# Optimization experiments

Hardware: AMD Instinct MI355X
Metric: run time of the kernel (lower is better)

## Reference

```python
import jax, jax.numpy as jnp
import numpy as np

NUM_HEADS = 12  # from init_kwargs


def setup_inputs() -> dict:
    key = jax.random.key(0)
    k1, k2, k3 = jax.random.split(key, 3)
    B, N, C = 8, 4096, 768
    x = jax.random.normal(k1, (B, N, C), dtype=jnp.float32)
    qkv_w = jax.random.normal(k2, (3 * C, C), dtype=jnp.float32) * (C ** -0.5)
    proj_w = jax.random.normal(k3, (C, C), dtype=jnp.float32) * (C ** -0.5)
    proj_b = jnp.zeros((C,), dtype=jnp.float32)
    return {"x": x, "qkv_w": qkv_w, "proj_w": proj_w, "proj_b": proj_b}


def reference(x, qkv_w, proj_w, proj_b):
    B, N, C = x.shape
    H = NUM_HEADS
    hd = C // H
    h = w = int(round(N ** 0.5))  # spatial grid, N = h*w
    # fused qkv projection (q, k are produced but never consumed, as in source)
    qkv = jnp.einsum('bnc,dc->bnd', x, qkv_w)          # [B, N, 3C]
    qkv = qkv.reshape(B, N, 3, H, hd)
    v = qkv[:, :, 2].transpose(0, 2, 1, 3)             # [B, H, N, hd]
    v2d = v.reshape(B, H, h, w, hd)
    # fft2 over spatial dims; concat(real, imag) then slice[:hd] == real part
    v_real = jnp.fft.fft2(v2d.astype(jnp.float32), axes=(2, 3)).real
    out = v_real.reshape(B, H, N, hd).transpose(0, 2, 1, 3).reshape(B, N, C)
    return jnp.einsum('bnc,dc->bnd', out, proj_w) + proj_b
```

## Files before the change

### kernel.cpp

```cpp
#include <hip/hip_runtime.h>
#include <hip/hip_bf16.h>


typedef __bf16 bf16x8 __attribute__((ext_vector_type(8)));
typedef __bf16 bf16x4 __attribute__((ext_vector_type(4)));
typedef float f32x4 __attribute__((ext_vector_type(4)));
typedef unsigned short ushort_t;
typedef unsigned int uint_t;

typedef __attribute__((address_space(3))) unsigned int lds_u32;
typedef __attribute__((address_space(1))) unsigned int glob_u32;

__device__ __forceinline__ void gl_lds16(const void* g, void* l) {
  __builtin_amdgcn_global_load_lds((const glob_u32*)g, (lds_u32*)l, 16, 0, 0);
}

__device__ __forceinline__ ushort_t f2bf(float f) {
  union { __hip_bfloat16 h; ushort_t s; } cv;
  cv.h = __float2bfloat16(f);
  return cv.s;
}

__device__ __forceinline__ bf16x8 ld_frag(const ushort_t* p) {
  union { bf16x8 v; bf16x4 h[2]; } r;
  r.h[0] = *(const bf16x4*)p;
  r.h[1] = *(const bf16x4*)(p + 4);
  return r.v;
}

__device__ __forceinline__ bf16x8 tw_frag(int m, int k0, bool use_sin, float sign) {
  union { bf16x8 v; ushort_t u[8]; } r;
#pragma unroll
  for (int j = 0; j < 8; ++j) {
    int ph = (m * (k0 + j)) & 63;
    float a = (float)ph * 0.09817477042468104f;
    float x = use_sin ? __sinf(a) : __cosf(a);
    r.u[j] = f2bf(sign * x);
  }
  return r.v;
}

__global__ __launch_bounds__(256) void precompute_mfma(const float* __restrict__ P,
                                                       const float* __restrict__ Q,
                                                       __hip_bfloat16* __restrict__ Mb) {
  __shared__ ushort_t As[128 * 40];
  __shared__ ushort_t Bs[128 * 36];
  const int t = threadIdx.x;
  const int i0 = blockIdx.y * 128, c0 = blockIdx.x * 128;
  const int w = t >> 6, l = t & 63;
  const int wm = w & 1, wn = w >> 1;
  const int lm = l & 15, lq = l >> 4;
  f32x4 acc[4][4] = {};
  for (int kt = 0; kt < 24; ++kt) {
    const int k0 = kt * 32;
    {
      int e = t * 16, row = e >> 5, dc = e & 16;
      const float* src = &P[(size_t)(i0 + row) * 768 + k0 + dc];
      float4 f0 = *(const float4*)&src[0], f1 = *(const float4*)&src[4];
      float4 f2 = *(const float4*)&src[8], f3 = *(const float4*)&src[12];
      union { ushort_t u[8]; uint4 v; } pk0, pk1;
      pk0.u[0] = f2bf(f0.x); pk0.u[1] = f2bf(f0.y); pk0.u[2] = f2bf(f0.z); pk0.u[3] = f2bf(f0.w);
      pk0.u[4] = f2bf(f1.x); pk0.u[5] = f2bf(f1.y); pk0.u[6] = f2bf(f1.z); pk0.u[7] = f2bf(f1.w);
      pk1.u[0] = f2bf(f2.x); pk1.u[1] = f2bf(f2.y); pk1.u[2] = f2bf(f2.z); pk1.u[3] = f2bf(f2.w);
      pk1.u[4] = f2bf(f3.x); pk1.u[5] = f2bf(f3.y); pk1.u[6] = f2bf(f3.z); pk1.u[7] = f2bf(f3.w);
      *(uint4*)&As[row * 40 + dc] = pk0.v;
      *(uint4*)&As[row * 40 + dc + 8] = pk1.v;
    }
#pragma unroll
    for (int it = 0; it < 8; ++it) {
      int p = it * 256 + t, c = p & 127, pr = p >> 7;
      float a = Q[(size_t)(1536 + k0 + 2 * pr) * 768 + c0 + c];
      float b = Q[(size_t)(1536 + k0 + 2 * pr + 1) * 768 + c0 + c];
      union { ushort_t u[2]; uint_t w_; } pk;
      pk.u[0] = f2bf(a); pk.u[1] = f2bf(b);
      *(uint_t*)&Bs[c * 36 + 2 * pr] = pk.w_;
    }
    __syncthreads();
    bf16x8 af[4], bfr[4];
#pragma unroll
    for (int mt = 0; mt < 4; ++mt)
      af[mt] = ld_frag(&As[(wm * 64 + mt * 16 + lm) * 40 + lq * 8]);
#pragma unroll
    for (int nt = 0; nt < 4; ++nt)
      bfr[nt] = ld_frag(&Bs[(wn * 64 + nt * 16 + lm) * 36 + lq * 8]);
#pragma unroll
    for (int mt = 0; mt < 4; ++mt)
#pragma unroll
      for (int nt = 0; nt < 4; ++nt)
        acc[mt][nt] = __builtin_amdgcn_mfma_f32_16x16x32_bf16(af[mt], bfr[nt], acc[mt][nt], 0, 0, 0);
    __syncthreads();
  }
#pragma unroll
  for (int nt = 0; nt < 4; ++nt) {
    const int col = c0 + wn * 64 + nt * 16 + lm;
#pragma unroll
    for (int mt = 0; mt < 4; ++mt) {
      const int rbase = i0 + wm * 64 + mt * 16 + lq * 4;
#pragma unroll
      for (int r = 0; r < 4; ++r)
        Mb[(size_t)(rbase + r) * 768 + col] = __float2bfloat16(acc[mt][nt][r]);
    }
  }
}

__global__ __launch_bounds__(256) void fft_a_mfma(const float* __restrict__ X,
                                                  __hip_bfloat16* __restrict__ Ar,
                                                  __hip_bfloat16* __restrict__ Ai) {
  __shared__ ushort_t Xs[128 * 68];
  __shared__ ushort_t Ep[48 * 136];
  const int t = threadIdx.x;
  const int s = blockIdx.y;
  const int c0 = blockIdx.x * 128;
  const float* src = X + (size_t)s * 64 * 768 + c0;
#pragma unroll
  for (int it = 0; it < 16; ++it) {
    int p = it * 256 + t;
    int c = p & 127, pr = p >> 7;
    float a = src[(size_t)(2 * pr) * 768 + c];
    float b = src[(size_t)(2 * pr + 1) * 768 + c];
    union { ushort_t u[2]; uint_t w_; } pk;
    pk.u[0] = f2bf(a); pk.u[1] = f2bf(b);
    *(uint_t*)&Xs[c * 68 + 2 * pr] = pk.w_;
  }
  __syncthreads();
  const int w = t >> 6, l = t & 63;
  const int lm = l & 15, lq = l >> 4;
  bf16x8 afc[3][2], afs[3][2];
#pragma unroll
  for (int mt = 0; mt < 3; ++mt)
#pragma unroll
    for (int ks = 0; ks < 2; ++ks) {
      int m = mt * 16 + lm;
      int k0 = ks * 32 + lq * 8;
      afc[mt][ks] = tw_frag(m, k0, false, 1.f);
      afs[mt][ks] = tw_frag(m, k0, true, 1.f);
    }
  f32x4 accr[3][2] = {}, acci[3][2] = {};
#pragma unroll
  for (int ks = 0; ks < 2; ++ks) {
    bf16x8 bf[2];
#pragma unroll
    for (int nt = 0; nt < 2; ++nt) {
      int c = w * 32 + nt * 16 + lm;
      bf[nt] = ld_frag(&Xs[c * 68 + ks * 32 + lq * 8]);
    }
#pragma unroll
    for (int mt = 0; mt < 3; ++mt)
#pragma unroll
      for (int nt = 0; nt < 2; ++nt) {
        accr[mt][nt] = __builtin_amdgcn_mfma_f32_16x16x32_bf16(afc[mt][ks], bf[nt], accr[mt][nt], 0, 0, 0);
        acci[mt][nt] = __builtin_amdgcn_mfma_f32_16x16x32_bf16(afs[mt][ks], bf[nt], acci[mt][nt], 0, 0, 0);
      }
  }
#pragma unroll
  for (int arr = 0; arr < 2; ++arr) {
    __syncthreads();
#pragma unroll
    for (int mt = 0; mt < 3; ++mt)
#pragma unroll
      for (int nt = 0; nt < 2; ++nt)
#pragma unroll
        for (int r = 0; r < 4; ++r) {
          int row = mt * 16 + lq * 4 + r;
          int col = w * 32 + nt * 16 + lm;
          float v = arr ? acci[mt][nt][r] : accr[mt][nt][r];
          Ep[row * 136 + col] = f2bf(v);
        }
    __syncthreads();
    __hip_bfloat16* dst = arr ? Ai : Ar;
#pragma unroll
    for (int it = 0; it < 3; ++it) {
      int idx = it * 256 + t;
      int row = idx >> 4, cq = (idx & 15) * 8;
      if (row <= 32) {
        uint4 v = *(const uint4*)&Ep[row * 136 + cq];
        *(uint4*)&dst[(size_t)(s * 64 + row) * 768 + c0 + cq] = v;
      }
    }
  }
}

__global__ __launch_bounds__(256) void fft_b_mfma(const __hip_bfloat16* __restrict__ Ar,
                                                  const __hip_bfloat16* __restrict__ Ai,
                                                  __hip_bfloat16* __restrict__ Xf) {
  __shared__ ushort_t Rs[128 * 68], Is[128 * 68];
  __shared__ ushort_t Ep[64 * 136];
  const int t = threadIdx.x;
  const int bz = blockIdx.y;
  const int b = bz / 33, k2 = bz % 33;
  const int c0 = blockIdx.x * 128;
  const ushort_t* ar = (const ushort_t*)Ar + ((size_t)(b * 64) * 64 + k2) * 768 + c0;
  const ushort_t* ai = (const ushort_t*)Ai + ((size_t)(b * 64) * 64 + k2) * 768 + c0;
  const size_t n1s = (size_t)64 * 768;
#pragma unroll
  for (int it = 0; it < 16; ++it) {
    int p = it * 256 + t;
    int c = p & 127, pr = p >> 7;
    size_t o0 = (size_t)(2 * pr) * n1s + c;
    size_t o1 = o0 + n1s;
    union { ushort_t u[2]; uint_t w_; } p1, p2;
    p1.u[0] = ar[o0]; p1.u[1] = ar[o1];
    p2.u[0] = ai[o0]; p2.u[1] = ai[o1];
    *(uint_t*)&Rs[c * 68 + 2 * pr] = p1.w_;
    *(uint_t*)&Is[c * 68 + 2 * pr] = p2.w_;
  }
  __syncthreads();
  const int w = t >> 6, l = t & 63;
  const int wm = w & 1, wn = w >> 1;
  const int lm = l & 15, lq = l >> 4;
  bf16x8 afc[2][2], afs[2][2];
#pragma unroll
  for (int mt = 0; mt < 2; ++mt)
#pragma unroll
    for (int ks = 0; ks < 2; ++ks) {
      int m = wm * 32 + mt * 16 + lm;
      int k0 = ks * 32 + lq * 8;
      afc[mt][ks] = tw_frag(m, k0, false, 1.f);
      afs[mt][ks] = tw_frag(m, k0, true, 1.f);
    }
  f32x4 accC[2][4] = {}, accS[2][4] = {};
#pragma unroll
  for (int ks = 0; ks < 2; ++ks) {
    bf16x8 bR[4], bI[4];
#pragma unroll
    for (int nt = 0; nt < 4; ++nt) {
      int c = wn * 64 + nt * 16 + lm;
      int kb = ks * 32 + lq * 8;
      bR[nt] = ld_frag(&Rs[c * 68 + kb]);
      bI[nt] = ld_frag(&Is[c * 68 + kb]);
    }
#pragma unroll
    for (int mt = 0; mt < 2; ++mt)
#pragma unroll
      for (int nt = 0; nt < 4; ++nt) {
        accC[mt][nt] = __builtin_amdgcn_mfma_f32_16x16x32_bf16(afc[mt][ks], bR[nt], accC[mt][nt], 0, 0, 0);
        accS[mt][nt] = __builtin_amdgcn_mfma_f32_16x16x32_bf16(afs[mt][ks], bI[nt], accS[mt][nt], 0, 0, 0);
      }
  }
  const int nout = (k2 >= 1 && k2 <= 31) ? 2 : 1;
  for (int o = 0; o < nout; ++o) {
    __syncthreads();
#pragma unroll
    for (int mt = 0; mt < 2; ++mt)
#pragma unroll
      for (int nt = 0; nt < 4; ++nt)
#pragma unroll
        for (int r = 0; r < 4; ++r) {
          int row = wm * 32 + mt * 16 + lq * 4 + r;
          int col = wn * 64 + nt * 16 + lm;
          float v = o ? (accC[mt][nt][r] + accS[mt][nt][r])
                      : (accC[mt][nt][r] - accS[mt][nt][r]);
          Ep[row * 136 + col] = f2bf(v);
        }
    __syncthreads();
    const int k2o = o ? (64 - k2) : k2;
#pragma unroll
    for (int it = 0; it < 4; ++it) {
      int idx = it * 256 + t;
      int k1 = idx >> 4, cq = (idx & 15) * 8;
      uint4 v = *(const uint4*)&Ep[k1 * 136 + cq];
      *(uint4*)&Xf[((size_t)b * 4096 + k1 * 64 + k2o) * 768 + c0 + cq] = v;
    }
  }
}

__global__ __launch_bounds__(256) void gemm_bt(const __hip_bfloat16* __restrict__ A,
                                               const __hip_bfloat16* __restrict__ B,
                                               const float* __restrict__ bias,
                                               float* __restrict__ C) {
  __shared__ __hip_bfloat16 As[128 * 32];
  __shared__ __hip_bfloat16 Bs[128 * 32];
  const int t = threadIdx.x, w = t >> 6, l = t & 63;
  const int L = blockIdx.x + blockIdx.y * 6;
  const int s = L >> 3, xcd = L & 7;
  const int n0 = (s % 6) * 128;
  const int m0 = ((s / 6) * 8 + xcd) * 128;
  const int wm = w & 1, wn = w >> 1;
  f32x4 acc[4][4] = {};
  const int srow_b = (l >> 2);
  const int scol = (l & 3) * 8;
  for (int kt = 0; kt < 24; ++kt) {
    const int k0 = kt * 32;
#pragma unroll
    for (int j = 0; j < 2; ++j) {
      const int ldso = (w * 2 + j) * 512;
      const int row = (w * 2 + j) * 16 + srow_b;
      gl_lds16(&A[(size_t)(m0 + row) * 768 + k0 + scol], &As[ldso]);
      gl_lds16(&B[(size_t)(n0 + row) * 768 + k0 + scol], &Bs[ldso]);
    }
    __syncthreads();
    bf16x8 af[4], bfr[4];
#pragma unroll
    for (int mt = 0; mt < 4; ++mt)
      af[mt] = *(const bf16x8*)&As[(wm * 64 + mt * 16 + (l & 15)) * 32 + (l >> 4) * 8];
#pragma unroll
    for (int nt = 0; nt < 4; ++nt)
      bfr[nt] = *(const bf16x8*)&Bs[(wn * 64 + nt * 16 + (l & 15)) * 32 + (l >> 4) * 8];
#pragma unroll
    for (int mt = 0; mt < 4; ++mt)
#pragma unroll
      for (int nt = 0; nt < 4; ++nt)
        acc[mt][nt] = __builtin_amdgcn_mfma_f32_16x16x32_bf16(af[mt], bfr[nt], acc[mt][nt], 0, 0, 0);
    __syncthreads();
  }
#pragma unroll
  for (int nt = 0; nt < 4; ++nt) {
    const int col = n0 + wn * 64 + nt * 16 + (l & 15);
    const float bv = bias[col];
#pragma unroll
    for (int mt = 0; mt < 4; ++mt) {
      const int rbase = m0 + wm * 64 + mt * 16 + (l >> 4) * 4;
#pragma unroll
      for (int r = 0; r < 4; ++r)
        C[(size_t)(rbase + r) * 768 + col] = acc[mt][nt][r] + bv;
    }
  }
}

extern "C" void kernel_launch(void* const* d_in, const int* in_sizes, int n_in,
                              void* d_out, int out_size, void* d_ws, size_t ws_size,
                              hipStream_t stream) {
  const float* x      = (const float*)d_in[0];
  const float* qkv_w  = (const float*)d_in[1];
  const float* proj_w = (const float*)d_in[2];
  const float* proj_b = (const float*)d_in[3];
  float* out = (float*)d_out;

  char* ws = (char*)d_ws;
  const size_t MB_BYTES = (size_t)768 * 768 * 2;
  const size_t ARR_BYTES = (size_t)8 * 4096 * 768 * 2;
  __hip_bfloat16* Mb = (__hip_bfloat16*)ws;
  __hip_bfloat16* Ar = (__hip_bfloat16*)(ws + MB_BYTES);
  __hip_bfloat16* Ai = (__hip_bfloat16*)(ws + MB_BYTES + ARR_BYTES);
  __hip_bfloat16* Xf = (__hip_bfloat16*)(ws + MB_BYTES + 2 * ARR_BYTES);

  precompute_mfma<<<dim3(6, 6), 256, 0, stream>>>(proj_w, qkv_w, Mb);
  fft_a_mfma<<<dim3(6, 512), 256, 0, stream>>>(x, Ar, Ai);
  fft_b_mfma<<<dim3(6, 264), 256, 0, stream>>>(Ar, Ai, Xf);
  gemm_bt<<<dim3(6, 256), 256, 0, stream>>>(Xf, Mb, proj_b, out);
}
```

Before: 310.2 us.

## Merge weight precompute into FFT stage, alias LDS, switch GEMM to 32x32 MFMA

The weight-product precompute kernel is folded into the first FFT kernel as extra blocks, removing one launch and letting the small GEMM overlap with FFT work. Both FFT kernels now alias their staging and epilogue LDS buffers to cut shared memory use and raise occupancy. The final GEMM moves to BK=64 tiles with an XOR-swizzled LDS layout and 32x32x16 MFMA, halving K iterations and barriers. The tradeoff is that the merged precompute blocks are long-running and may become a tail within the FFT grid.

```diff
diff --git a/kernel.cpp b/kernel.cpp
--- a/kernel.cpp
+++ b/kernel.cpp
@@ -5,6 +5,7 @@
 typedef __bf16 bf16x8 __attribute__((ext_vector_type(8)));
 typedef __bf16 bf16x4 __attribute__((ext_vector_type(4)));
 typedef float f32x4 __attribute__((ext_vector_type(4)));
+typedef float f32x16 __attribute__((ext_vector_type(16)));
 typedef unsigned short ushort_t;
 typedef unsigned int uint_t;
 
@@ -40,141 +41,141 @@
   return r.v;
 }
 
-__global__ __launch_bounds__(256) void precompute_mfma(const float* __restrict__ P,
-                                                       const float* __restrict__ Q,
-                                                       __hip_bfloat16* __restrict__ Mb) {
-  __shared__ ushort_t As[128 * 40];
-  __shared__ ushort_t Bs[128 * 36];
+__global__ __launch_bounds__(256) void fft_a_pre(const float* __restrict__ X,
+                                                 const float* __restrict__ P,
+                                                 const float* __restrict__ Q,
+                                                 __hip_bfloat16* __restrict__ Ar,
+                                                 __hip_bfloat16* __restrict__ Ai,
+                                                 __hip_bfloat16* __restrict__ Mb) {
+  __shared__ ushort_t smem[9728];
   const int t = threadIdx.x;
-  const int i0 = blockIdx.y * 128, c0 = blockIdx.x * 128;
+  const int c0 = blockIdx.x * 128;
   const int w = t >> 6, l = t & 63;
-  const int wm = w & 1, wn = w >> 1;
   const int lm = l & 15, lq = l >> 4;
-  f32x4 acc[4][4] = {};
-  for (int kt = 0; kt < 24; ++kt) {
-    const int k0 = kt * 32;
-    {
-      int e = t * 16, row = e >> 5, dc = e & 16;
-      const float* src = &P[(size_t)(i0 + row) * 768 + k0 + dc];
-      float4 f0 = *(const float4*)&src[0], f1 = *(const float4*)&src[4];
-      float4 f2 = *(const float4*)&src[8], f3 = *(const float4*)&src[12];
-      union { ushort_t u[8]; uint4 v; } pk0, pk1;
-      pk0.u[0] = f2bf(f0.x); pk0.u[1] = f2bf(f0.y); pk0.u[2] = f2bf(f0.z); pk0.u[3] = f2bf(f0.w);
-      pk0.u[4] = f2bf(f1.x); pk0.u[5] = f2bf(f1.y); pk0.u[6] = f2bf(f1.z); pk0.u[7] = f2bf(f1.w);
-      pk1.u[0] = f2bf(f2.x); pk1.u[1] = f2bf(f2.y); pk1.u[2] = f2bf(f2.z); pk1.u[3] = f2bf(f2.w);
-      pk1.u[4] = f2bf(f3.x); pk1.u[5] = f2bf(f3.y); pk1.u[6] = f2bf(f3.z); pk1.u[7] = f2bf(f3.w);
-      *(uint4*)&As[row * 40 + dc] = pk0.v;
-      *(uint4*)&As[row * 40 + dc + 8] = pk1.v;
-    }
-#pragma unroll
-    for (int it = 0; it < 8; ++it) {
-      int p = it * 256 + t, c = p & 127, pr = p >> 7;
-      float a = Q[(size_t)(1536 + k0 + 2 * pr) * 768 + c0 + c];
-      float b = Q[(size_t)(1536 + k0 + 2 * pr + 1) * 768 + c0 + c];
+
+  if (blockIdx.y < 512) {
+    ushort_t* Xs = smem;
+    ushort_t* Ep = smem;
+    const int s = blockIdx.y;
+    const float* src = X + (size_t)s * 64 * 768 + c0;
+#pragma unroll
+    for (int it = 0; it < 16; ++it) {
+      int p = it * 256 + t;
+      int c = p & 127, pr = p >> 7;
+      float a = src[(size_t)(2 * pr) * 768 + c];
+      float b = src[(size_t)(2 * pr + 1) * 768 + c];
       union { ushort_t u[2]; uint_t w_; } pk;
       pk.u[0] = f2bf(a); pk.u[1] = f2bf(b);
-      *(uint_t*)&Bs[c * 36 + 2 * pr] = pk.w_;
-    }
-    __syncthreads();
-    bf16x8 af[4], bfr[4];
-#pragma unroll
-    for (int mt = 0; mt < 4; ++mt)
-      af[mt] = ld_frag(&As[(wm * 64 + mt * 16 + lm) * 40 + lq * 8]);
-#pragma unroll
-    for (int nt = 0; nt < 4; ++nt)
-      bfr[nt] = ld_frag(&Bs[(wn * 64 + nt * 16 + lm) * 36 + lq * 8]);
-#pragma unroll
-    for (int mt = 0; mt < 4; ++mt)
+      *(uint_t*)&Xs[c * 68 + 2 * pr] = pk.w_;
+    }
+    __syncthreads();
+    bf16x8 afc[3][2], afs[3][2];
+#pragma unroll
+    for (int mt = 0; mt < 3; ++mt)
+#pragma unroll
+      for (int ks = 0; ks < 2; ++ks) {
+        int m = mt * 16 + lm;
+        int k0 = ks * 32 + lq * 8;
+        afc[mt][ks] = tw_frag(m, k0, false, 1.f);
+        afs[mt][ks] = tw_frag(m, k0, true, 1.f);
+      }
+    f32x4 accr[3][2] = {}, acci[3][2] = {};
+#pragma unroll
+    for (int ks = 0; ks < 2; ++ks) {
+      bf16x8 bf[2];
+#pragma unroll
+      for (int nt = 0; nt < 2; ++nt) {
+        int c = w * 32 + nt * 16 + lm;
+        bf[nt] = ld_frag(&Xs[c * 68 + ks * 32 + lq * 8]);
+      }
+#pragma unroll
+      for (int mt = 0; mt < 3; ++mt)
+#pragma unroll
+        for (int nt = 0; nt < 2; ++nt) {
+          accr[mt][nt] = __builtin_amdgcn_mfma_f32_16x16x32_bf16(afc[mt][ks], bf[nt], accr[mt][nt], 0, 0, 0);
+          acci[mt][nt] = __builtin_amdgcn_mfma_f32_16x16x32_bf16(afs[mt][ks], bf[nt], acci[mt][nt], 0, 0, 0);
+        }
+    }
+#pragma unroll
+    for (int arr = 0; arr < 2; ++arr) {
+      __syncthreads();
+#pragma unroll
+      for (int mt = 0; mt < 3; ++mt)
+#pragma unroll
+        for (int nt = 0; nt < 2; ++nt)
+#pragma unroll
+          for (int r = 0; r < 4; ++r) {
+            int row = mt * 16 + lq * 4 + r;
+            int col = w * 32 + nt * 16 + lm;
+            float v = arr ? acci[mt][nt][r] : accr[mt][nt][r];
+            Ep[row * 136 + col] = f2bf(v);
+          }
+      __syncthreads();
+      __hip_bfloat16* dst = arr ? Ai : Ar;
+#pragma unroll
+      for (int it = 0; it < 3; ++it) {
+        int idx = it * 256 + t;
+        int row = idx >> 4, cq = (idx & 15) * 8;
+        if (row <= 32) {
+          uint4 v = *(const uint4*)&Ep[row * 136 + cq];
+          *(uint4*)&dst[(size_t)(s * 64 + row) * 768 + c0 + cq] = v;
+        }
+      }
+    }
+  } else {
+    ushort_t* As = smem;
+    ushort_t* Bs = smem + 5120;
+    const int i0 = (blockIdx.y - 512) * 128;
+    const int wm = w & 1, wn = w >> 1;
+    f32x4 acc[4][4] = {};
+    for (int kt = 0; kt < 24; ++kt) {
+      const int k0 = kt * 32;
+      {
+        int e = t * 16, row = e >> 5, dc = e & 16;
+        const float* src = &P[(size_t)(i0 + row) * 768 + k0 + dc];
+        float4 f0 = *(const float4*)&src[0], f1 = *(const float4*)&src[4];
+        float4 f2 = *(const float4*)&src[8], f3 = *(const float4*)&src[12];
+        union { ushort_t u[8]; uint4 v; } pk0, pk1;
+        pk0.u[0] = f2bf(f0.x); pk0.u[1] = f2bf(f0.y); pk0.u[2] = f2bf(f0.z); pk0.u[3] = f2bf(f0.w);
+        pk0.u[4] = f2bf(f1.x); pk0.u[5] = f2bf(f1.y); pk0.u[6] = f2bf(f1.z); pk0.u[7] = f2bf(f1.w);
+        pk1.u[0] = f2bf(f2.x); pk1.u[1] = f2bf(f2.y); pk1.u[2] = f2bf(f2.z); pk1.u[3] = f2bf(f2.w);
+        pk1.u[4] = f2bf(f3.x); pk1.u[5] = f2bf(f3.y); pk1.u[6] = f2bf(f3.z); pk1.u[7] = f2bf(f3.w);
+        *(uint4*)&As[row * 40 + dc] = pk0.v;
+        *(uint4*)&As[row * 40 + dc + 8] = pk1.v;
+      }
+#pragma unroll
+      for (int it = 0; it < 8; ++it) {
+        int p = it * 256 + t, c = p & 127, pr = p >> 7;
+        float a = Q[(size_t)(1536 + k0 + 2 * pr) * 768 + c0 + c];
+        float b = Q[(size_t)(1536 + k0 + 2 * pr + 1) * 768 + c0 + c];
+        union { ushort_t u[2]; uint_t w_; } pk;
+        pk.u[0] = f2bf(a); pk.u[1] = f2bf(b);
+        *(uint_t*)&Bs[c * 36 + 2 * pr] = pk.w_;
+      }
+      __syncthreads();
+      bf16x8 af[4], bfr[4];
+#pragma unroll
+      for (int mt = 0; mt < 4; ++mt)
+        af[mt] = ld_frag(&As[(wm * 64 + mt * 16 + lm) * 40 + lq * 8]);
 #pragma unroll
       for (int nt = 0; nt < 4; ++nt)
-        acc[mt][nt] = __builtin_amdgcn_mfma_f32_16x16x32_bf16(af[mt], bfr[nt], acc[mt][nt], 0, 0, 0);
-    __syncthreads();
-  }
-#pragma unroll
-  for (int nt = 0; nt < 4; ++nt) {
-    const int col = c0 + wn * 64 + nt * 16 + lm;
-#pragma unroll
-    for (int mt = 0; mt < 4; ++mt) {
-      const int rbase = i0 + wm * 64 + mt * 16 + lq * 4;
-#pragma unroll
-      for (int r = 0; r < 4; ++r)
-        Mb[(size_t)(rbase + r) * 768 + col] = __float2bfloat16(acc[mt][nt][r]);
-    }
-  }
-}
-
-__global__ __launch_bounds__(256) void fft_a_mfma(const float* __restrict__ X,
-                                                  __hip_bfloat16* __restrict__ Ar,
-                                                  __hip_bfloat16* __restrict__ Ai) {
-  __shared__ ushort_t Xs[128 * 68];
-  __shared__ ushort_t Ep[48 * 136];
-  const int t = threadIdx.x;
-  const int s = blockIdx.y;
-  const int c0 = blockIdx.x * 128;
-  const float* src = X + (size_t)s * 64 * 768 + c0;
-#pragma unroll
-  for (int it = 0; it < 16; ++it) {
-    int p = it * 256 + t;
-    int c = p & 127, pr = p >> 7;
-    float a = src[(size_t)(2 * pr) * 768 + c];
-    float b = src[(size_t)(2 * pr + 1) * 768 + c];
-    union { ushort_t u[2]; uint_t w_; } pk;
-    pk.u[0] = f2bf(a); pk.u[1] = f2bf(b);
-    *(uint_t*)&Xs[c * 68 + 2 * pr] = pk.w_;
-  }
-  __syncthreads();
-  const int w = t >> 6, l = t & 63;
-  const int lm = l & 15, lq = l >> 4;
-  bf16x8 afc[3][2], afs[3][2];
-#pragma unroll
-  for (int mt = 0; mt < 3; ++mt)
-#pragma unroll
-    for (int ks = 0; ks < 2; ++ks) {
-      int m = mt * 16 + lm;
-      int k0 = ks * 32 + lq * 8;
-      afc[mt][ks] = tw_frag(m, k0, false, 1.f);
-      afs[mt][ks] = tw_frag(m, k0, true, 1.f);
-    }
-  f32x4 accr[3][2] = {}, acci[3][2] = {};
-#pragma unroll
-  for (int ks = 0; ks < 2; ++ks) {
-    bf16x8 bf[2];
-#pragma unroll
-    for (int nt = 0; nt < 2; ++nt) {
-      int c = w * 32 + nt * 16 + lm;
-      bf[nt] = ld_frag(&Xs[c * 68 + ks * 32 + lq * 8]);
-    }
-#pragma unroll
-    for (int mt = 0; mt < 3; ++mt)
-#pragma unroll
-      for (int nt = 0; nt < 2; ++nt) {
-        accr[mt][nt] = __builtin_amdgcn_mfma_f32_16x16x32_bf16(afc[mt][ks], bf[nt], accr[mt][nt], 0, 0, 0);
-        acci[mt][nt] = __builtin_amdgcn_mfma_f32_16x16x32_bf16(afs[mt][ks], bf[nt], acci[mt][nt], 0, 0, 0);
-      }
-  }
-#pragma unroll
-  for (int arr = 0; arr < 2; ++arr) {
-    __syncthreads();
-#pragma unroll
-    for (int mt = 0; mt < 3; ++mt)
-#pragma unroll
-      for (int nt = 0; nt < 2; ++nt)
-#pragma unroll
-        for (int r = 0; r < 4; ++r) {
-          int row = mt * 16 + lq * 4 + r;
-          int col = w * 32 + nt * 16 + lm;
-          float v = arr ? acci[mt][nt][r] : accr[mt][nt][r];
-          Ep[row * 136 + col] = f2bf(v);
-        }
-    __syncthreads();
-    __hip_bfloat16* dst = arr ? Ai : Ar;
-#pragma unroll
-    for (int it = 0; it < 3; ++it) {
-      int idx = it * 256 + t;
-      int row = idx >> 4, cq = (idx & 15) * 8;
-      if (row <= 32) {
-        uint4 v = *(const uint4*)&Ep[row * 136 + cq];
-        *(uint4*)&dst[(size_t)(s * 64 + row) * 768 + c0 + cq] = v;
+        bfr[nt] = ld_frag(&Bs[(wn * 64 + nt * 16 + lm) * 36 + lq * 8]);
+#pragma unroll
+      for (int mt = 0; mt < 4; ++mt)
+#pragma unroll
+        for (int nt = 0; nt < 4; ++nt)
+          acc[mt][nt] = __builtin_amdgcn_mfma_f32_16x16x32_bf16(af[mt], bfr[nt], acc[mt][nt], 0, 0, 0);
+      __syncthreads();
+    }
+#pragma unroll
+    for (int nt = 0; nt < 4; ++nt) {
+      const int col = c0 + wn * 64 + nt * 16 + lm;
+#pragma unroll
+      for (int mt = 0; mt < 4; ++mt) {
+        const int rbase = i0 + wm * 64 + mt * 16 + lq * 4;
+#pragma unroll
+        for (int r = 0; r < 4; ++r)
+          Mb[(size_t)(rbase + r) * 768 + col] = __float2bfloat16(acc[mt][nt][r]);
       }
     }
   }
@@ -183,8 +184,10 @@
 __global__ __launch_bounds__(256) void fft_b_mfma(const __hip_bfloat16* __restrict__ Ar,
                                                   const __hip_bfloat16* __restrict__ Ai,
                                                   __hip_bfloat16* __restrict__ Xf) {
-  __shared__ ushort_t Rs[128 * 68], Is[128 * 68];
-  __shared__ ushort_t Ep[64 * 136];
+  __shared__ ushort_t smem[17408];
+  ushort_t* Rs = smem;
+  ushort_t* Is = smem + 8704;
+  ushort_t* Ep = smem;
   const int t = threadIdx.x;
   const int bz = blockIdx.y;
   const int b = bz / 33, k2 = bz % 33;
@@ -268,51 +271,63 @@
                                                const __hip_bfloat16* __restrict__ B,
                                                const float* __restrict__ bias,
                                                float* __restrict__ C) {
-  __shared__ __hip_bfloat16 As[128 * 32];
-  __shared__ __hip_bfloat16 Bs[128 * 32];
+  __shared__ ushort_t As[128 * 64];
+  __shared__ ushort_t Bs[128 * 64];
   const int t = threadIdx.x, w = t >> 6, l = t & 63;
   const int L = blockIdx.x + blockIdx.y * 6;
   const int s = L >> 3, xcd = L & 7;
   const int n0 = (s % 6) * 128;
   const int m0 = ((s / 6) * 8 + xcd) * 128;
   const int wm = w & 1, wn = w >> 1;
-  f32x4 acc[4][4] = {};
-  const int srow_b = (l >> 2);
-  const int scol = (l & 3) * 8;
-  for (int kt = 0; kt < 24; ++kt) {
-    const int k0 = kt * 32;
-#pragma unroll
-    for (int j = 0; j < 2; ++j) {
-      const int ldso = (w * 2 + j) * 512;
-      const int row = (w * 2 + j) * 16 + srow_b;
-      gl_lds16(&A[(size_t)(m0 + row) * 768 + k0 + scol], &As[ldso]);
-      gl_lds16(&B[(size_t)(n0 + row) * 768 + k0 + scol], &Bs[ldso]);
-    }
-    __syncthreads();
-    bf16x8 af[4], bfr[4];
-#pragma unroll
-    for (int mt = 0; mt < 4; ++mt)
-      af[mt] = *(const bf16x8*)&As[(wm * 64 + mt * 16 + (l & 15)) * 32 + (l >> 4) * 8];
-#pragma unroll
-    for (int nt = 0; nt < 4; ++nt)
-      bfr[nt] = *(const bf16x8*)&Bs[(wn * 64 + nt * 16 + (l & 15)) * 32 + (l >> 4) * 8];
-#pragma unroll
-    for (int mt = 0; mt < 4; ++mt)
-#pragma unroll
-      for (int nt = 0; nt < 4; ++nt)
-        acc[mt][nt] = __builtin_amdgcn_mfma_f32_16x16x32_bf16(af[mt], bfr[nt], acc[mt][nt], 0, 0, 0);
-    __syncthreads();
-  }
-#pragma unroll
-  for (int nt = 0; nt < 4; ++nt) {
-    const int col = n0 + wn * 64 + nt * 16 + (l & 15);
+  f32x16 acc[2][2] = {};
+  const int srow = l >> 3;
+  const int schunk = (l & 7) ^ srow;
+  const int lr = l & 31, lh = l >> 5;
+  for (int kt = 0; kt < 12; ++kt) {
+    const int k0 = kt * 64;
+#pragma unroll
+    for (int i = 0; i < 4; ++i) {
+      const int rbase = w * 32 + i * 8;
+      const int row = rbase + srow;
+      gl_lds16(&A[(size_t)(m0 + row) * 768 + k0 + schunk * 8], &As[rbase * 64]);
+      gl_lds16(&B[(size_t)(n0 + row) * 768 + k0 + schunk * 8], &Bs[rbase * 64]);
+    }
+    __syncthreads();
+#pragma unroll
+    for (int ks = 0; ks < 4; ++ks) {
+      bf16x8 af[2], bf[2];
+#pragma unroll
+      for (int mt = 0; mt < 2; ++mt) {
+        int row = wm * 64 + mt * 32 + lr;
+        int ch = (ks * 2 + lh) ^ (lr & 7);
+        af[mt] = *(const bf16x8*)&As[row * 64 + ch * 8];
+      }
+#pragma unroll
+      for (int nt = 0; nt < 2; ++nt) {
+        int row = wn * 64 + nt * 32 + lr;
+        int ch = (ks * 2 + lh) ^ (lr & 7);
+        bf[nt] = *(const bf16x8*)&Bs[row * 64 + ch * 8];
+      }
+#pragma unroll
+      for (int mt = 0; mt < 2; ++mt)
+#pragma unroll
+        for (int nt = 0; nt < 2; ++nt)
+          acc[mt][nt] = __builtin_amdgcn_mfma_f32_32x32x16_bf16(af[mt], bf[nt], acc[mt][nt], 0, 0, 0);
+    }
+    __syncthreads();
+  }
+#pragma unroll
+  for (int nt = 0; nt < 2; ++nt) {
+    const int col = n0 + wn * 64 + nt * 32 + lr;
     const float bv = bias[col];
 #pragma unroll
-    for (int mt = 0; mt < 4; ++mt) {
-      const int rbase = m0 + wm * 64 + mt * 16 + (l >> 4) * 4;
-#pragma unroll
-      for (int r = 0; r < 4; ++r)
-        C[(size_t)(rbase + r) * 768 + col] = acc[mt][nt][r] + bv;
+    for (int mt = 0; mt < 2; ++mt) {
+      const int rb = m0 + wm * 64 + mt * 32 + 4 * lh;
+#pragma unroll
+      for (int reg = 0; reg < 16; ++reg) {
+        const int row = rb + (reg & 3) + 8 * (reg >> 2);
+        C[(size_t)row * 768 + col] = acc[mt][nt][reg] + bv;
+      }
     }
   }
 }
@@ -334,8 +349,7 @@
   __hip_bfloat16* Ai = (__hip_bfloat16*)(ws + MB_BYTES + ARR_BYTES);
   __hip_bfloat16* Xf = (__hip_bfloat16*)(ws + MB_BYTES + 2 * ARR_BYTES);
 
-  precompute_mfma<<<dim3(6, 6), 256, 0, stream>>>(proj_w, qkv_w, Mb);
-  fft_a_mfma<<<dim3(6, 512), 256, 0, stream>>>(x, Ar, Ai);
+  fft_a_pre<<<dim3(6, 518), 256, 0, stream>>>(x, proj_w, qkv_w, Ar, Ai, Mb);
   fft_b_mfma<<<dim3(6, 264), 256, 0, stream>>>(Ar, Ai, Xf);
   gemm_bt<<<dim3(6, 256), 256, 0, stream>>>(Xf, Mb, proj_b, out);
 }
```

New measurement: 280.6 us. -9.6%, faster.
